# Performance work log

Hardware: AMD Instinct MI355X
Metric: run time of the kernel (lower is better)

Reference implementation:

```python
import jax, jax.numpy as jnp
import numpy as np

N_NODES = 100000
N_EDGES = 1200000
IN_DIM = 64
OUT_DIM = 64
LN_EPS = 1e-5


def setup_inputs() -> dict:
    key = jax.random.key(0)
    k_x, k_e, k_w, k_b, k_g, k_beta = jax.random.split(key, 6)
    x = jax.random.normal(k_x, (N_NODES, IN_DIM), dtype=jnp.float32)
    edge_index = jax.random.randint(k_e, (2, N_EDGES), 0, N_NODES, dtype=jnp.int64)
    # nn.Linear(in_dim*2, out_dim): weight [out, 2*in], bias [out]
    lim = 1.0 / np.sqrt(2 * IN_DIM)
    W = jax.random.uniform(k_w, (OUT_DIM, 2 * IN_DIM), minval=-lim, maxval=lim, dtype=jnp.float32)
    b = jax.random.uniform(k_b, (OUT_DIM,), minval=-lim, maxval=lim, dtype=jnp.float32)
    gamma = jnp.ones((OUT_DIM,), dtype=jnp.float32)
    beta = jnp.zeros((OUT_DIM,), dtype=jnp.float32)
    return {"x": x, "W": W, "b": b, "gamma": gamma, "beta": beta, "edge_index": edge_index}


def reference(x, W, b, gamma, beta, edge_index):
    i = edge_index[0]  # destination nodes (aggregation target)
    j = edge_index[1]  # source nodes (neighbor features)
    n = x.shape[0]
    # mean aggregation: scatter-add gathered neighbor feats, divide by degree
    agg = jax.ops.segment_sum(x[j], i, num_segments=n)  # [N, in_dim]
    deg = jax.ops.segment_sum(jnp.ones(i.shape, x.dtype), i, num_segments=n)
    agg = agg / jnp.maximum(deg, 1.0)[:, None]
    # concat + linear + relu
    h = jnp.concatenate([x, agg], axis=-1) @ W.T + b  # [N, out_dim]
    h = jax.nn.relu(h)
    # layernorm (dropout p=0 is identity in eval)
    mu = jnp.mean(h, axis=-1, keepdims=True)
    var = jnp.var(h, axis=-1, keepdims=True)
    return (h - mu) / jnp.sqrt(var + LN_EPS) * gamma + beta
```

## Files before the change

### kernel.cpp

```cpp
#include <hip/hip_runtime.h>
#include <hip/hip_bf16.h>

#define N_NODES 100000
#define N_EDGES 1200000
#define LN_EPS 1e-5f
#define CAP 40
#define NBIN 782
#define BINW 128
#define BCAP 1792
#define EPB 4096
#define P1_BLOCKS 293
#define CONV_BLOCKS 507
#define NSTRIDE 42
#define NBLK2 1563

typedef __attribute__((ext_vector_type(8))) short short8;
typedef __attribute__((ext_vector_type(8))) unsigned short us8;
typedef __attribute__((ext_vector_type(4))) float float4v;
typedef __attribute__((ext_vector_type(2))) int   ivec2;

__device__ __forceinline__ short bfb(float v) {
    __hip_bfloat16 h = __float2bfloat16(v);
    short s; __builtin_memcpy(&s, &h, 2); return s;
}
__device__ __forceinline__ float b2f(unsigned short u) {
    unsigned int xi = ((unsigned int)u) << 16;
    float f; __builtin_memcpy(&f, &xi, 4); return f;
}

__global__ __launch_bounds__(256) void k_bin3(
    const float* __restrict__ x, unsigned short* __restrict__ xb,
    const int* __restrict__ ei, int* __restrict__ btail,
    int* __restrict__ binbuf)
{
    const int tid = threadIdx.x;

    if (blockIdx.x >= P1_BLOCKS) {
        for (int i = (blockIdx.x - P1_BLOCKS) * 256 + tid; i < N_NODES * 8;
             i += CONV_BLOCKS * 256) {
            float4v f0 = *(const float4v*)(x + 8 * i);
            float4v f1 = *(const float4v*)(x + 8 * i + 4);
            short8 p;
            p[0] = bfb(f0.x); p[1] = bfb(f0.y); p[2] = bfb(f0.z); p[3] = bfb(f0.w);
            p[4] = bfb(f1.x); p[5] = bfb(f1.y); p[6] = bfb(f1.z); p[7] = bfb(f1.w);
            *(short8*)(xb + 8 * i) = p;
        }
        return;
    }

    __shared__ int   bcnt[NBIN];
    __shared__ int   bbase[NBIN];
    __shared__ int   bgbase[NBIN];
    __shared__ int   bfill[NBIN];
    __shared__ int   scanbuf[256];
    __shared__ ivec2 stage[EPB];

    for (int i = tid; i < NBIN; i += 256) { bcnt[i] = 0; bfill[i] = 0; }
    __syncthreads();

    const int ebase = blockIdx.x * EPB;
    int d[16], s[16];
#pragma unroll
    for (int u = 0; u < 16; ++u) {
        int e = ebase + u * 256 + tid;
        bool v = (e < N_EDGES);
        d[u] = v ? ei[e] : -1;
        s[u] = v ? ei[N_EDGES + e] : 0;
        if (v) atomicAdd(&bcnt[d[u] >> 7], 1);
    }
    __syncthreads();

    int v4[4], tsum = 0;
#pragma unroll
    for (int k = 0; k < 4; ++k) {
        int b = 4 * tid + k;
        v4[k] = (b < NBIN) ? bcnt[b] : 0;
        tsum += v4[k];
    }
    scanbuf[tid] = tsum;
    __syncthreads();
    for (int off = 1; off < 256; off <<= 1) {
        int t = (tid >= off) ? scanbuf[tid - off] : 0;
        __syncthreads();
        scanbuf[tid] += t;
        __syncthreads();
    }
    int run = scanbuf[tid] - tsum;
#pragma unroll
    for (int k = 0; k < 4; ++k) {
        int b = 4 * tid + k;
        if (b < NBIN) bbase[b] = run;
        run += v4[k];
    }
    const int tot = scanbuf[255];

    for (int b = tid; b < NBIN; b += 256) {
        int c = bcnt[b];
        bgbase[b] = c ? atomicAdd(&btail[b], c) : 0;
    }
    __syncthreads();

#pragma unroll
    for (int u = 0; u < 16; ++u) {
        if (d[u] >= 0) {
            int b = d[u] >> 7;
            int p = bbase[b] + atomicAdd(&bfill[b], 1);
            stage[p] = (ivec2){d[u], s[u]};
        }
    }
    __syncthreads();

    for (int i = tid; i < tot; i += 256) {
        ivec2 e = stage[i];
        int b = e.x >> 7;
        int pos = bgbase[b] + (i - bbase[b]);
        if (pos < BCAP)
            binbuf[(size_t)b * BCAP + pos] = ((e.x & 127) << 17) | e.y;
    }
}

__global__ __launch_bounds__(256, 4) void node_fused(
    const unsigned short* __restrict__ xb,
    const int* __restrict__ btail, const int* __restrict__ binbuf,
    const float* __restrict__ W, const float* __restrict__ bias,
    const float* __restrict__ gamma, const float* __restrict__ beta,
    float* __restrict__ out)
{
    __shared__ short Wl[64 * 136];
    __shared__ int   nlist[64 * NSTRIDE];
    __shared__ int   lcnt[64];

    const int tid = threadIdx.x;
    const int bin  = blockIdx.x >> 1;
    const int half = blockIdx.x & 1;
    const int nodebase = blockIdx.x * 64;

    for (int i = tid; i < 64 * 64; i += 256) {
        int row = i >> 6, cp = i & 63;
        const float* wr = W + row * 128 + cp * 2;
        short2 v; v.x = bfb(wr[0]); v.y = bfb(wr[1]);
        *(short2*)&Wl[row * 136 + cp * 2] = v;
    }
    if (tid < 64) lcnt[tid] = 0;
    __syncthreads();

    const int nb = min(btail[bin], BCAP);
    for (int i = tid; i < nb; i += 256) {
        int pk = binbuf[(size_t)bin * BCAP + i];
        int nl = (pk >> 17) - (half << 6);
        if ((unsigned)nl < 64u) {
            int slot = atomicAdd(&lcnt[nl], 1);
            if (slot < CAP) nlist[nl * NSTRIDE + slot] = pk & 0x1FFFF;
        }
    }
    __syncthreads();

    const int wid  = tid >> 6;
    const int lane = tid & 63;
    const int g    = lane >> 4;
    const int c    = lane & 15;
    const int ch   = c & 7;
    const int pr   = c >> 3;
    const int nbase = nodebase + wid * 16;
    if (nbase >= N_NODES) return;

    int dfull[4], dgs[4];
#pragma unroll
    for (int r = 0; r < 4; ++r) {
        dfull[r] = lcnt[wid * 16 + r * 4 + g];
        dgs[r]   = min(dfull[r], CAP);
    }
    float aa[4][8];
#pragma unroll
    for (int r = 0; r < 4; ++r)
#pragma unroll
        for (int k = 0; k < 8; ++k) aa[r][k] = 0.0f;

    const int dmax = max(max(dgs[0], dgs[1]), max(dgs[2], dgs[3]));
    for (int t = 0; t < dmax; t += 8) {
#pragma unroll
        for (int u = 0; u < 4; ++u) {
#pragma unroll
            for (int r = 0; r < 4; ++r) {
                int idx = t + 2 * u + pr;
                if (idx < dgs[r]) {
                    int j = nlist[(wid * 16 + r * 4 + g) * NSTRIDE + idx];
                    us8 v = *(const us8*)(xb + (size_t)j * 64 + ch * 8);
#pragma unroll
                    for (int k = 0; k < 8; ++k) aa[r][k] += b2f(v[k]);
                }
            }
        }
    }

    const unsigned short* xrow = xb + (size_t)(nbase + c) * 64 + g * 8;
    short8 A0 = *(const short8*)(xrow);
    short8 A1 = *(const short8*)(xrow + 32);

#pragma unroll
    for (int r = 0; r < 4; ++r)
#pragma unroll
        for (int k = 0; k < 8; ++k) aa[r][k] += __shfl_xor(aa[r][k], 8);

    short* aL = (short*)&nlist[wid * 16 * NSTRIDE];
#pragma unroll
    for (int r = 0; r < 4; ++r) {
        float rd = 1.0f / fmaxf((float)dfull[r], 1.0f);
        int m = r * 4 + g;
        short8 p;
#pragma unroll
        for (int k = 0; k < 8; ++k) p[k] = bfb(aa[r][k] * rd);
        if (pr == 0)
            *(short8*)(aL + m * 72 + ch * 8) = p;
    }
    short8 A2 = *(const short8*)(aL + c * 72 + g * 8);
    short8 A3 = *(const short8*)(aL + c * 72 + 32 + g * 8);

    float bs_[4], gm_[4], bt_[4];
#pragma unroll
    for (int ct = 0; ct < 4; ++ct) {
        bs_[ct] = bias[ct * 16 + c];
        gm_[ct] = gamma[ct * 16 + c];
        bt_[ct] = beta[ct * 16 + c];
    }

    float4v acc[4];
#pragma unroll
    for (int ct = 0; ct < 4; ++ct) {
        float bb = bs_[ct];
        acc[ct] = (float4v){bb, bb, bb, bb};
    }
#pragma unroll
    for (int ks = 0; ks < 4; ++ks) {
        short8 Af = (ks == 0) ? A0 : (ks == 1) ? A1 : (ks == 2) ? A2 : A3;
#pragma unroll
        for (int ct = 0; ct < 4; ++ct) {
            short8 Bf = *(const short8*)(Wl + (ct * 16 + c) * 136 + ks * 32 + g * 8);
            acc[ct] = __builtin_amdgcn_mfma_f32_16x16x32_bf16(Af, Bf, acc[ct], 0, 0, 0);
        }
    }

    float s_[4] = {0, 0, 0, 0}, q_[4] = {0, 0, 0, 0};
#pragma unroll
    for (int ct = 0; ct < 4; ++ct)
#pragma unroll
        for (int r = 0; r < 4; ++r) {
            float h = fmaxf(acc[ct][r], 0.0f);
            acc[ct][r] = h;
            s_[r] += h;
            q_[r] += h * h;
        }
#pragma unroll
    for (int off = 1; off <= 8; off <<= 1)
#pragma unroll
        for (int r = 0; r < 4; ++r) {
            s_[r] += __shfl_xor(s_[r], off);
            q_[r] += __shfl_xor(q_[r], off);
        }
#pragma unroll
    for (int r = 0; r < 4; ++r) {
        float mu = s_[r] * (1.0f / 64.0f);
        float var = q_[r] * (1.0f / 64.0f) - mu * mu;
        float is = rsqrtf(var + LN_EPS);
        int node = nbase + g * 4 + r;
        if (node < N_NODES) {
#pragma unroll
            for (int ct = 0; ct < 4; ++ct) {
                out[node * 64 + ct * 16 + c] =
                    (acc[ct][r] - mu) * is * gm_[ct] + bt_[ct];
            }
        }
    }
}

extern "C" void kernel_launch(void* const* d_in, const int* in_sizes, int n_in,
                              void* d_out, int out_size, void* d_ws, size_t ws_size,
                              hipStream_t stream) {
    const float* x     = (const float*)d_in[0];
    const float* W     = (const float*)d_in[1];
    const float* b     = (const float*)d_in[2];
    const float* gamma = (const float*)d_in[3];
    const float* beta  = (const float*)d_in[4];
    const int*   ei    = (const int*)d_in[5];
    float* out = (float*)d_out;

    int* btail = (int*)d_ws;
    int* binbuf = (int*)((char*)d_ws + 4096);
    unsigned short* xb = (unsigned short*)(binbuf + (size_t)NBIN * BCAP);

    (void)hipMemsetAsync(btail, 0, NBIN * sizeof(int), stream);

    k_bin3<<<P1_BLOCKS + CONV_BLOCKS, 256, 0, stream>>>(x, xb, ei, btail, binbuf);
    node_fused<<<NBLK2, 256, 0, stream>>>(xb, btail, binbuf, W, b, gamma, beta, out);
}
```

Before: 150.9 us.

## Replace block-local binning with direct global-atomic edge scatter; deepen gather unroll

The shared-memory counting sort that grouped edges per bin before a coalesced write is replaced by a simple kernel where each thread loads 4 edges and claims slots with global atomicAdd on per-bin tails. This removes the block scan, the LDS staging and several barriers, at the cost of about 1.2M global atomics on only 782 counters and scattered writes. The node kernel now loads 32 neighbor indices up front per 16-wide step so more gather loads can be in flight, and raises the launch-bounds occupancy hint from 4 to 5 blocks.

```diff
diff --git a/kernel.cpp b/kernel.cpp
--- a/kernel.cpp
+++ b/kernel.cpp
@@ -8,15 +8,15 @@
 #define NBIN 782
 #define BINW 128
 #define BCAP 1792
-#define EPB 4096
-#define P1_BLOCKS 293
-#define CONV_BLOCKS 507
 #define NSTRIDE 42
 #define NBLK2 1563
+#define SCAT_BLOCKS 1172
+#define CONV2 507
 
 typedef __attribute__((ext_vector_type(8))) short short8;
 typedef __attribute__((ext_vector_type(8))) unsigned short us8;
 typedef __attribute__((ext_vector_type(4))) float float4v;
+typedef __attribute__((ext_vector_type(4))) int   ivec4;
 typedef __attribute__((ext_vector_type(2))) int   ivec2;
 
 __device__ __forceinline__ short bfb(float v) {
@@ -28,16 +28,16 @@
     float f; __builtin_memcpy(&f, &xi, 4); return f;
 }
 
-__global__ __launch_bounds__(256) void k_bin3(
+__global__ __launch_bounds__(256) void k_scatter(
     const float* __restrict__ x, unsigned short* __restrict__ xb,
     const int* __restrict__ ei, int* __restrict__ btail,
     int* __restrict__ binbuf)
 {
     const int tid = threadIdx.x;
 
-    if (blockIdx.x >= P1_BLOCKS) {
-        for (int i = (blockIdx.x - P1_BLOCKS) * 256 + tid; i < N_NODES * 8;
-             i += CONV_BLOCKS * 256) {
+    if (blockIdx.x >= SCAT_BLOCKS) {
+        for (int i = (blockIdx.x - SCAT_BLOCKS) * 256 + tid; i < N_NODES * 8;
+             i += CONV2 * 256) {
             float4v f0 = *(const float4v*)(x + 8 * i);
             float4v f1 = *(const float4v*)(x + 8 * i + 4);
             short8 p;
@@ -48,78 +48,22 @@
         return;
     }
 
-    __shared__ int   bcnt[NBIN];
-    __shared__ int   bbase[NBIN];
-    __shared__ int   bgbase[NBIN];
-    __shared__ int   bfill[NBIN];
-    __shared__ int   scanbuf[256];
-    __shared__ ivec2 stage[EPB];
-
-    for (int i = tid; i < NBIN; i += 256) { bcnt[i] = 0; bfill[i] = 0; }
-    __syncthreads();
-
-    const int ebase = blockIdx.x * EPB;
-    int d[16], s[16];
-#pragma unroll
-    for (int u = 0; u < 16; ++u) {
-        int e = ebase + u * 256 + tid;
-        bool v = (e < N_EDGES);
-        d[u] = v ? ei[e] : -1;
-        s[u] = v ? ei[N_EDGES + e] : 0;
-        if (v) atomicAdd(&bcnt[d[u] >> 7], 1);
-    }
-    __syncthreads();
-
-    int v4[4], tsum = 0;
-#pragma unroll
-    for (int k = 0; k < 4; ++k) {
-        int b = 4 * tid + k;
-        v4[k] = (b < NBIN) ? bcnt[b] : 0;
-        tsum += v4[k];
-    }
-    scanbuf[tid] = tsum;
-    __syncthreads();
-    for (int off = 1; off < 256; off <<= 1) {
-        int t = (tid >= off) ? scanbuf[tid - off] : 0;
-        __syncthreads();
-        scanbuf[tid] += t;
-        __syncthreads();
-    }
-    int run = scanbuf[tid] - tsum;
-#pragma unroll
-    for (int k = 0; k < 4; ++k) {
-        int b = 4 * tid + k;
-        if (b < NBIN) bbase[b] = run;
-        run += v4[k];
-    }
-    const int tot = scanbuf[255];
-
-    for (int b = tid; b < NBIN; b += 256) {
-        int c = bcnt[b];
-        bgbase[b] = c ? atomicAdd(&btail[b], c) : 0;
-    }
-    __syncthreads();
-
-#pragma unroll
-    for (int u = 0; u < 16; ++u) {
-        if (d[u] >= 0) {
-            int b = d[u] >> 7;
-            int p = bbase[b] + atomicAdd(&bfill[b], 1);
-            stage[p] = (ivec2){d[u], s[u]};
-        }
-    }
-    __syncthreads();
-
-    for (int i = tid; i < tot; i += 256) {
-        ivec2 e = stage[i];
-        int b = e.x >> 7;
-        int pos = bgbase[b] + (i - bbase[b]);
-        if (pos < BCAP)
-            binbuf[(size_t)b * BCAP + pos] = ((e.x & 127) << 17) | e.y;
-    }
-}
-
-__global__ __launch_bounds__(256, 4) void node_fused(
+    const int e4 = (blockIdx.x * 256 + tid) * 4;
+    if (e4 < N_EDGES) {
+        ivec4 d4 = *(const ivec4*)(ei + e4);
+        ivec4 s4 = *(const ivec4*)(ei + N_EDGES + e4);
+#pragma unroll
+        for (int u = 0; u < 4; ++u) {
+            int d = d4[u], s = s4[u];
+            int bin = d >> 7;
+            int slot = atomicAdd(&btail[bin], 1);
+            if (slot < BCAP)
+                binbuf[(size_t)bin * BCAP + slot] = ((d & 127) << 17) | s;
+        }
+    }
+}
+
+__global__ __launch_bounds__(256, 5) void node_fused(
     const unsigned short* __restrict__ xb,
     const int* __restrict__ btail, const int* __restrict__ binbuf,
     const float* __restrict__ W, const float* __restrict__ bias,
@@ -165,10 +109,12 @@
     if (nbase >= N_NODES) return;
 
     int dfull[4], dgs[4];
+    const int* nrow[4];
 #pragma unroll
     for (int r = 0; r < 4; ++r) {
         dfull[r] = lcnt[wid * 16 + r * 4 + g];
         dgs[r]   = min(dfull[r], CAP);
+        nrow[r]  = &nlist[(wid * 16 + r * 4 + g) * NSTRIDE];
     }
     float aa[4][8];
 #pragma unroll
@@ -177,20 +123,26 @@
         for (int k = 0; k < 8; ++k) aa[r][k] = 0.0f;
 
     const int dmax = max(max(dgs[0], dgs[1]), max(dgs[2], dgs[3]));
-    for (int t = 0; t < dmax; t += 8) {
-#pragma unroll
-        for (int u = 0; u < 4; ++u) {
+    for (int t = 0; t < dmax; t += 16) {
+        int jj[32];
+#pragma unroll
+        for (int u = 0; u < 8; ++u)
 #pragma unroll
             for (int r = 0; r < 4; ++r) {
                 int idx = t + 2 * u + pr;
-                if (idx < dgs[r]) {
-                    int j = nlist[(wid * 16 + r * 4 + g) * NSTRIDE + idx];
+                jj[u * 4 + r] = (idx < dgs[r]) ? nrow[r][idx] : -1;
+            }
+#pragma unroll
+        for (int u = 0; u < 8; ++u)
+#pragma unroll
+            for (int r = 0; r < 4; ++r) {
+                int j = jj[u * 4 + r];
+                if (j >= 0) {
                     us8 v = *(const us8*)(xb + (size_t)j * 64 + ch * 8);
 #pragma unroll
                     for (int k = 0; k < 8; ++k) aa[r][k] += b2f(v[k]);
                 }
             }
-        }
     }
 
     const unsigned short* xrow = xb + (size_t)(nbase + c) * 64 + g * 8;
@@ -290,6 +242,6 @@
 
     (void)hipMemsetAsync(btail, 0, NBIN * sizeof(int), stream);
 
-    k_bin3<<<P1_BLOCKS + CONV_BLOCKS, 256, 0, stream>>>(x, xb, ei, btail, binbuf);
+    k_scatter<<<SCAT_BLOCKS + CONV2, 256, 0, stream>>>(x, xb, ei, btail, binbuf);
     node_fused<<<NBLK2, 256, 0, stream>>>(xb, btail, binbuf, W, b, gamma, beta, out);
 }
```

Measured after the change: 440.4 us. +191.8%, slower.
